# Kernel tuning notes

Measured on AMD Instinct MI355X. Metric: run time of the kernel, lower is better.

Reference implementation:

```python
import jax, jax.numpy as jnp
import numpy as np

BOUND = 25   # max decode steps (module's `bound`)
SOS = 1      # start-of-sequence token index


def setup_inputs() -> dict:
    key = jax.random.key(0)
    ks = jax.random.split(key, 8)
    H, A, D, V, S = 1024, 1024, 512, 50257, 128
    def rn(k, shape, s=0.02):
        return jax.random.normal(k, shape, dtype=jnp.float32) * s
    return {
        "hidden": rn(ks[0], (1, 1, H), 1.0),        # [n_layers, batch=1, H]
        "embeddings": rn(ks[1], (1, S, A), 1.0),    # encoder states [1, S, A]
        "E": rn(ks[2], (V, D)),                      # word embedding table
        "W_ih": rn(ks[3], (3 * H, D)),               # GRU input weights (r,z,n)
        "W_hh": rn(ks[4], (3 * H, H)),               # GRU hidden weights
        "b_ih": jnp.zeros((3 * H,), jnp.float32),
        "b_hh": jnp.zeros((3 * H,), jnp.float32),
        "Wq": rn(ks[5], (A, H)),                     # attention query projection H->A
        "Wout": rn(ks[6], (V, A + H)),               # output projection
        "bout": jnp.zeros((V,), jnp.float32),
    }


def _decode(hidden, embeddings, E, W_ih, W_hh, b_ih, b_hh, Wq, Wout, bout):
    h0 = hidden[-1]  # [1, H] — last-layer hidden (n_layers=1)

    def step(carry, _):
        h, word = carry                      # h: [1,H], word: [1] int32
        x = E[word]                          # [1, D]  (dropout = identity at eval)
        gi = x @ W_ih.T + b_ih               # [1, 3H]
        gh = h @ W_hh.T + b_hh               # [1, 3H]
        ir, iz, inn = jnp.split(gi, 3, axis=-1)
        hr, hz, hn = jnp.split(gh, 3, axis=-1)
        r = jax.nn.sigmoid(ir + hr)
        z = jax.nn.sigmoid(iz + hz)
        n = jnp.tanh(inn + r * hn)
        h_new = (1.0 - z) * n + z * h        # GRU cell (torch gate order r,z,n)
        q = h_new @ Wq.T                     # [1, A] attention query
        scores = jnp.einsum('bsa,ba->bs', embeddings, q)      # [1, S]
        w = jax.nn.softmax(scores, axis=-1)
        attn = jnp.einsum('bs,bsa->ba', w, embeddings)        # [1, A]
        merge = jnp.concatenate([h_new, attn], axis=-1)       # [1, H+A]
        lp = jax.nn.log_softmax(merge @ Wout.T + bout, axis=-1)  # [1, V]
        nw = jnp.argmax(lp, axis=-1).astype(jnp.int32)        # greedy (topk k=1)
        return (h_new, nw), (lp[0], w[0], nw[0])

    word0 = jnp.array([SOS], dtype=jnp.int32)
    _, (log_probs, weights, tokens) = jax.lax.scan(step, (h0, word0), None, length=BOUND)
    # log_probs: [BOUND, V], weights: [BOUND, S], tokens: [BOUND]
    return log_probs, weights, tokens


def reference(hidden, embeddings, E, W_ih, W_hh, b_ih, b_hh, Wq, Wout, bout):
    return _decode(hidden, embeddings, E, W_ih, W_hh, b_ih, b_hh, Wq, Wout, bout)
```

## Files before the change

### kernel.cpp

```cpp
#include <hip/hip_runtime.h>
#include <hip/hip_fp16.h>
#include <math.h>

#define Hh 1024
#define Dd 512
#define Aa 1024
#define Vv 50257
#define Ss 128
#define NSTEP 25

#define OFF_H      0
#define OFF_GI     1024
#define OFF_GH     4096
#define OFF_MERGE  7168
#define OFF_Q      9216
#define OFF_LOGITS 10368
#define OFF_PM     60625
#define OFF_PL     60689
#define OFF_PI     60753
#define OFF_WORD   60818

#define WOUTH_BYTE_OFF (1u << 20)
#define NG_CONV (50257u * 256u)

__global__ void k_conv(const float4* __restrict__ src, uint4* __restrict__ dst, unsigned n8) {
    unsigned stride = gridDim.x * blockDim.x;
    for (unsigned g = blockIdx.x * blockDim.x + threadIdx.x; g < n8; g += stride) {
        float4 a = src[(size_t)g * 2], b = src[(size_t)g * 2 + 1];
        union { __half2 h[4]; uint4 u; } pk;
        pk.h[0] = __float22half2_rn(make_float2(a.x, a.y));
        pk.h[1] = __float22half2_rn(make_float2(a.z, a.w));
        pk.h[2] = __float22half2_rn(make_float2(b.x, b.y));
        pk.h[3] = __float22half2_rn(make_float2(b.z, b.w));
        dst[g] = pk.u;
    }
}

__global__ void k_init(const float* __restrict__ hidden, float* __restrict__ ws) {
    int i = blockIdx.x * blockDim.x + threadIdx.x;
    if (i < Hh) ws[OFF_H + i] = hidden[i];
    if (i == 0) ((int*)ws)[OFF_WORD] = 1;
}

__global__ void k_gates(const float* __restrict__ E, const float* __restrict__ W_ih,
                        const float* __restrict__ W_hh, const float* __restrict__ b_ih,
                        const float* __restrict__ b_hh, float* __restrict__ ws) {
    int gwave = (blockIdx.x * blockDim.x + threadIdx.x) >> 6;
    int lane = threadIdx.x & 63;
    if (gwave >= 3 * Hh) return;
    int word = ((const int*)ws)[OFF_WORD];
    const float4* x  = (const float4*)(E + (size_t)word * Dd);
    const float4* h  = (const float4*)(ws + OFF_H);
    const float4* wi = (const float4*)(W_ih + (size_t)gwave * Dd);
    const float4* wh = (const float4*)(W_hh + (size_t)gwave * Hh);
    float accI = 0.f, accH = 0.f;
    #pragma unroll
    for (int it = 0; it < 2; it++) {
        int k = it * 64 + lane;
        float4 a = wi[k], b = x[k];
        accI += a.x * b.x + a.y * b.y + a.z * b.z + a.w * b.w;
    }
    #pragma unroll
    for (int it = 0; it < 4; it++) {
        int k = it * 64 + lane;
        float4 a = wh[k], b = h[k];
        accH += a.x * b.x + a.y * b.y + a.z * b.z + a.w * b.w;
    }
    for (int off = 32; off; off >>= 1) {
        accI += __shfl_down(accI, off);
        accH += __shfl_down(accH, off);
    }
    if (lane == 0) {
        ws[OFF_GI + gwave] = accI + b_ih[gwave];
        ws[OFF_GH + gwave] = accH + b_hh[gwave];
    }
}

__global__ void k_update(float* __restrict__ ws) {
    int i = blockIdx.x * blockDim.x + threadIdx.x;
    if (i >= Hh) return;
    float ir = ws[OFF_GI + i], iz = ws[OFF_GI + Hh + i], inn = ws[OFF_GI + 2 * Hh + i];
    float hr = ws[OFF_GH + i], hz = ws[OFF_GH + Hh + i], hn  = ws[OFF_GH + 2 * Hh + i];
    float r = 1.f / (1.f + expf(-(ir + hr)));
    float z = 1.f / (1.f + expf(-(iz + hz)));
    float n = tanhf(inn + r * hn);
    float h = ws[OFF_H + i];
    float hnew = (1.f - z) * n + z * h;
    ws[OFF_H + i] = hnew;
    ws[OFF_MERGE + i] = hnew;
}

__global__ void k_query(const float* __restrict__ Wq, float* __restrict__ ws) {
    int gwave = (blockIdx.x * blockDim.x + threadIdx.x) >> 6;
    int lane = threadIdx.x & 63;
    if (gwave >= Aa) return;
    const float4* h = (const float4*)(ws + OFF_H);
    const float4* w = (const float4*)(Wq + (size_t)gwave * Hh);
    float acc = 0.f;
    #pragma unroll
    for (int it = 0; it < 4; it++) {
        int k = it * 64 + lane;
        float4 a = w[k], b = h[k];
        acc += a.x * b.x + a.y * b.y + a.z * b.z + a.w * b.w;
    }
    for (int off = 32; off; off >>= 1) acc += __shfl_down(acc, off);
    if (lane == 0) ws[OFF_Q + gwave] = acc;
}

__global__ void k_scores_attn(const float* __restrict__ emb, float* __restrict__ ws,
                              float* __restrict__ outw) {
    __shared__ float sc[Ss];
    __shared__ float red[4];
    int t = threadIdx.x, wave = t >> 6, lane = t & 63;
    const float4* q = (const float4*)(ws + OFF_Q);
    for (int s = wave; s < Ss; s += 4) {
        const float4* e = (const float4*)(emb + (size_t)s * Aa);
        float acc = 0.f;
        #pragma unroll
        for (int it = 0; it < 4; it++) {
            int k = it * 64 + lane;
            float4 a = e[k], b = q[k];
            acc += a.x * b.x + a.y * b.y + a.z * b.z + a.w * b.w;
        }
        for (int off = 32; off; off >>= 1) acc += __shfl_down(acc, off);
        if (lane == 0) sc[s] = acc;
    }
    __syncthreads();
    float v = (t < Ss) ? sc[t] : -1e30f;
    float m = v;
    for (int off = 32; off; off >>= 1) m = fmaxf(m, __shfl_down(m, off));
    if (lane == 0) red[wave] = m;
    __syncthreads();
    float mm = fmaxf(fmaxf(red[0], red[1]), fmaxf(red[2], red[3]));
    __syncthreads();
    float e = (t < Ss) ? expf(v - mm) : 0.f;
    float sum = e;
    for (int off = 32; off; off >>= 1) sum += __shfl_down(sum, off);
    if (lane == 0) red[wave] = sum;
    __syncthreads();
    float ssum = red[0] + red[1] + red[2] + red[3];
    __syncthreads();
    if (t < Ss) {
        float w = e / ssum;
        sc[t] = w;
        outw[t] = w;
    }
    __syncthreads();
    for (int a = t; a < Aa; a += 256) {
        float acc = 0.f;
        for (int s = 0; s < Ss; s++) acc += sc[s] * emb[(size_t)s * Aa + a];
        ws[OFF_MERGE + Hh + a] = acc;
    }
}

__global__ void k_logits(const uint4* __restrict__ WoutH, const float* __restrict__ bout,
                         float* __restrict__ ws) {
    __shared__ float4 sm[512];
    const float4* mg = (const float4*)(ws + OFF_MERGE);
    for (int i = threadIdx.x; i < 512; i += blockDim.x) sm[i] = mg[i];
    __syncthreads();
    int wave = threadIdx.x >> 6, lane = threadIdx.x & 63;
    int row = blockIdx.x * 4 + wave;
    if (row >= Vv) return;
    const uint4* wr = WoutH + (size_t)row * 256;
    float acc = 0.f;
    #pragma unroll
    for (int it = 0; it < 4; it++) {
        int k = it * 64 + lane;
        union { uint4 u; __half2 h[4]; } pk;
        pk.u = wr[k];
        float4 m0 = sm[k * 2], m1 = sm[k * 2 + 1];
        float2 f0 = __half22float2(pk.h[0]);
        float2 f1 = __half22float2(pk.h[1]);
        float2 f2 = __half22float2(pk.h[2]);
        float2 f3 = __half22float2(pk.h[3]);
        acc += f0.x * m0.x + f0.y * m0.y + f1.x * m0.z + f1.y * m0.w
             + f2.x * m1.x + f2.y * m1.y + f3.x * m1.z + f3.y * m1.w;
    }
    for (int off = 32; off; off >>= 1) acc += __shfl_down(acc, off);
    if (lane == 0) ws[OFF_LOGITS + row] = acc + bout[row];
}

__global__ void k_reduce1(float* __restrict__ ws) {
    const float* logits = ws + OFF_LOGITS;
    __shared__ float smax[256], ssum[256];
    __shared__ int sidx[256];
    int t = threadIdx.x;
    int gid = blockIdx.x * 256 + t;
    float m = -1e30f, l = 0.f;
    int idx = 0;
    for (int i = gid; i < Vv; i += 64 * 256) {
        float v = logits[i];
        if (v > m) { l = l * expf(m - v) + 1.f; m = v; idx = i; }
        else       { l += expf(v - m); }
    }
    smax[t] = m; ssum[t] = l; sidx[t] = idx;
    __syncthreads();
    for (int stride = 128; stride; stride >>= 1) {
        if (t < stride) {
            float m1 = smax[t], l1 = ssum[t]; int i1 = sidx[t];
            float m2 = smax[t + stride], l2 = ssum[t + stride]; int i2 = sidx[t + stride];
            float M = fmaxf(m1, m2);
            float L = l1 * expf(m1 - M) + l2 * expf(m2 - M);
            int I = (m2 > m1) ? i2 : ((m2 < m1) ? i1 : min(i1, i2));
            smax[t] = M; ssum[t] = L; sidx[t] = I;
        }
        __syncthreads();
    }
    if (t == 0) {
        ws[OFF_PM + blockIdx.x] = smax[0];
        ws[OFF_PL + blockIdx.x] = ssum[0];
        ((int*)ws)[OFF_PI + blockIdx.x] = sidx[0];
    }
}

__global__ void k_final(float* __restrict__ ws, float* __restrict__ out_lp,
                        float* __restrict__ out_tok) {
    __shared__ float s_lse;
    int t = threadIdx.x;
    if (t < 64) {
        float m = ws[OFF_PM + t];
        float l = ws[OFF_PL + t];
        int idx = ((const int*)ws)[OFF_PI + t];
        for (int off = 32; off; off >>= 1) {
            float m2 = __shfl_down(m, off);
            float l2 = __shfl_down(l, off);
            int   i2 = __shfl_down(idx, off);
            float M = fmaxf(m, m2);
            float L = l * expf(m - M) + l2 * expf(m2 - M);
            int   I = (m2 > m) ? i2 : ((m2 < m) ? idx : min(idx, i2));
            m = M; l = L; idx = I;
        }
        if (t == 0) {
            s_lse = m + logf(l);
            if (blockIdx.x == 0) {
                ((int*)ws)[OFF_WORD] = idx;
                out_tok[0] = (float)idx;
            }
        }
    }
    __syncthreads();
    int i = blockIdx.x * 256 + t;
    if (i < Vv) out_lp[i] = ws[OFF_LOGITS + i] - s_lse;
}

extern "C" void kernel_launch(void* const* d_in, const int* in_sizes, int n_in,
                              void* d_out, int out_size, void* d_ws, size_t ws_size,
                              hipStream_t stream) {
    const float* hidden = (const float*)d_in[0];
    const float* emb    = (const float*)d_in[1];
    const float* E      = (const float*)d_in[2];
    const float* W_ih   = (const float*)d_in[3];
    const float* W_hh   = (const float*)d_in[4];
    const float* b_ih   = (const float*)d_in[5];
    const float* b_hh   = (const float*)d_in[6];
    const float* Wq     = (const float*)d_in[7];
    const float* Wout   = (const float*)d_in[8];
    const float* bout   = (const float*)d_in[9];

    float* ws = (float*)d_ws;
    uint4* WoutH = (uint4*)((char*)d_ws + WOUTH_BYTE_OFF);
    float* out_lp  = (float*)d_out;
    float* out_w   = out_lp + (size_t)NSTEP * Vv;
    float* out_tok = out_w + (size_t)NSTEP * Ss;

    k_conv<<<8192, 256, 0, stream>>>((const float4*)Wout, WoutH, NG_CONV);
    k_init<<<4, 256, 0, stream>>>(hidden, ws);
    for (int t = 0; t < NSTEP; t++) {
        k_gates      <<<768, 256, 0, stream>>>(E, W_ih, W_hh, b_ih, b_hh, ws);
        k_update     <<<4, 256, 0, stream>>>(ws);
        k_query      <<<256, 256, 0, stream>>>(Wq, ws);
        k_scores_attn<<<1, 256, 0, stream>>>(emb, ws, out_w + (size_t)t * Ss);
        k_logits     <<<(Vv + 3) / 4, 256, 0, stream>>>((const uint4*)WoutH, bout, ws);
        k_reduce1    <<<64, 256, 0, stream>>>(ws);
        k_final      <<<(Vv + 255) / 256, 256, 0, stream>>>(ws, out_lp + (size_t)t * Vv,
                                                            out_tok + t);
    }
}
```

Measured before the change: 2.503 ms.

## Fuse decode step kernels, fold Wq into encoder states, defer log-softmax normalization

Collapses the seven per-step kernels into three. The GRU gates and update are fused into one head kernel that also finishes the previous step's argmax/LSE reduction. The attention query projection is folded into a precomputed emb·Wq matrix, and the attention kernel is spread over eight blocks. Logits are written directly to the output with per-block online max/sum/argmax, and the LSE subtraction runs once for all steps in a final fixup kernel. This cuts launch count, drops one matmul per step and removes the separate logits buffer pass. The trade-offs are the extra one-time fold and fixup kernels, and the head kernel's reduction being redundantly computed by all 256 blocks.

```diff
diff --git a/kernel.cpp b/kernel.cpp
--- a/kernel.cpp
+++ b/kernel.cpp
@@ -9,19 +9,24 @@
 #define Ss 128
 #define NSTEP 25
 
-#define OFF_H      0
-#define OFF_GI     1024
-#define OFF_GH     4096
-#define OFF_MERGE  7168
-#define OFF_Q      9216
-#define OFF_LOGITS 10368
-#define OFF_PM     60625
-#define OFF_PL     60689
-#define OFF_PI     60753
-#define OFF_WORD   60818
+#define ROWS_PER_BLK 16
+#define NBLK_LOG ((Vv + ROWS_PER_BLK - 1) / ROWS_PER_BLK)
+
+#define OFF_H0     0
+#define OFF_H1     1024
+#define OFF_MERGE  2048
+#define OFF_PM     4096
+#define OFF_PL     8192
+#define OFF_PI     12288
+#define OFF_LSE    16384
+#define OFF_M      32768
 
 #define WOUTH_BYTE_OFF (1u << 20)
 #define NG_CONV (50257u * 256u)
+
+__device__ __forceinline__ float dot4(float4 a, float4 b) {
+    return a.x * b.x + a.y * b.y + a.z * b.z + a.w * b.w;
+}
 
 __global__ void k_conv(const float4* __restrict__ src, uint4* __restrict__ dst, unsigned n8) {
     unsigned stride = gridDim.x * blockDim.x;
@@ -36,212 +41,306 @@
     }
 }
 
+__global__ void k_fold(const float* __restrict__ emb, const float* __restrict__ Wq,
+                       float* __restrict__ ws) {
+    __shared__ float se[Aa];
+    int s = blockIdx.x;
+    for (int a = threadIdx.x; a < Aa; a += 256) se[a] = emb[(size_t)s * Aa + a];
+    __syncthreads();
+    int h = threadIdx.x;
+    float a0 = 0.f, a1 = 0.f, a2 = 0.f, a3 = 0.f;
+    for (int a = 0; a < Aa; a++) {
+        float e = se[a];
+        const float* wr = Wq + (size_t)a * Hh;
+        a0 += e * wr[h];
+        a1 += e * wr[h + 256];
+        a2 += e * wr[h + 512];
+        a3 += e * wr[h + 768];
+    }
+    float* Mrow = ws + OFF_M + (size_t)s * Hh;
+    Mrow[h] = a0; Mrow[h + 256] = a1; Mrow[h + 512] = a2; Mrow[h + 768] = a3;
+}
+
 __global__ void k_init(const float* __restrict__ hidden, float* __restrict__ ws) {
     int i = blockIdx.x * blockDim.x + threadIdx.x;
-    if (i < Hh) ws[OFF_H + i] = hidden[i];
-    if (i == 0) ((int*)ws)[OFF_WORD] = 1;
-}
-
-__global__ void k_gates(const float* __restrict__ E, const float* __restrict__ W_ih,
-                        const float* __restrict__ W_hh, const float* __restrict__ b_ih,
-                        const float* __restrict__ b_hh, float* __restrict__ ws) {
-    int gwave = (blockIdx.x * blockDim.x + threadIdx.x) >> 6;
-    int lane = threadIdx.x & 63;
-    if (gwave >= 3 * Hh) return;
-    int word = ((const int*)ws)[OFF_WORD];
-    const float4* x  = (const float4*)(E + (size_t)word * Dd);
-    const float4* h  = (const float4*)(ws + OFF_H);
-    const float4* wi = (const float4*)(W_ih + (size_t)gwave * Dd);
-    const float4* wh = (const float4*)(W_hh + (size_t)gwave * Hh);
-    float accI = 0.f, accH = 0.f;
+    if (i < Hh) ws[OFF_H0 + i] = hidden[i];
+}
+
+__global__ void k_head(int first, int par, int tprev,
+                       const float* __restrict__ E, const float* __restrict__ W_ih,
+                       const float* __restrict__ W_hh, const float* __restrict__ b_ih,
+                       const float* __restrict__ b_hh, float* __restrict__ ws,
+                       float* __restrict__ out_tok) {
+    __shared__ float sm_[256], sl_[256];
+    __shared__ int si_[256];
+    __shared__ int s_word;
+    int t = threadIdx.x;
+    int word;
+    if (first) {
+        word = 1;
+    } else {
+        const float* pm = ws + OFF_PM;
+        const float* pl = ws + OFF_PL;
+        const int* pi = (const int*)ws + OFF_PI;
+        float m = -1e30f, l = 0.f; int idx = 0x7fffffff;
+        for (int i = t; i < NBLK_LOG; i += 256) {
+            float m2 = pm[i], l2 = pl[i]; int i2 = pi[i];
+            float M = fmaxf(m, m2);
+            float L = l * expf(m - M) + l2 * expf(m2 - M);
+            idx = (m2 > m) ? i2 : ((m2 < m) ? idx : min(idx, i2));
+            m = M; l = L;
+        }
+        sm_[t] = m; sl_[t] = l; si_[t] = idx;
+        __syncthreads();
+        for (int s = 128; s; s >>= 1) {
+            if (t < s) {
+                float m1 = sm_[t], l1 = sl_[t]; int i1 = si_[t];
+                float m2 = sm_[t + s], l2 = sl_[t + s]; int i2 = si_[t + s];
+                float M = fmaxf(m1, m2);
+                sl_[t] = l1 * expf(m1 - M) + l2 * expf(m2 - M);
+                si_[t] = (m2 > m1) ? i2 : ((m2 < m1) ? i1 : min(i1, i2));
+                sm_[t] = M;
+            }
+            __syncthreads();
+        }
+        if (t == 0) {
+            s_word = si_[0];
+            if (blockIdx.x == 0) {
+                out_tok[tprev] = (float)si_[0];
+                ws[OFF_LSE + tprev] = sm_[0] + logf(sl_[0]);
+            }
+        }
+        __syncthreads();
+        word = s_word;
+    }
+
+    int lane = t & 63;
+    int row = blockIdx.x * 4 + (t >> 6);
+    const float* hprev = ws + (par ? OFF_H1 : OFF_H0);
+    float* hnext = ws + (par ? OFF_H0 : OFF_H1);
+    const float4* x4 = (const float4*)(E + (size_t)word * Dd);
+    const float4* h4 = (const float4*)hprev;
+    const float4* wir = (const float4*)(W_ih + (size_t)row * Dd);
+    const float4* wiz = (const float4*)(W_ih + (size_t)(Hh + row) * Dd);
+    const float4* win = (const float4*)(W_ih + (size_t)(2 * Hh + row) * Dd);
+    const float4* whr = (const float4*)(W_hh + (size_t)row * Hh);
+    const float4* whz = (const float4*)(W_hh + (size_t)(Hh + row) * Hh);
+    const float4* whn = (const float4*)(W_hh + (size_t)(2 * Hh + row) * Hh);
+    float aIr = 0.f, aIz = 0.f, aIn = 0.f, aHr = 0.f, aHz = 0.f, aHn = 0.f;
     #pragma unroll
     for (int it = 0; it < 2; it++) {
         int k = it * 64 + lane;
-        float4 a = wi[k], b = x[k];
-        accI += a.x * b.x + a.y * b.y + a.z * b.z + a.w * b.w;
+        float4 b = x4[k];
+        aIr += dot4(wir[k], b); aIz += dot4(wiz[k], b); aIn += dot4(win[k], b);
     }
     #pragma unroll
     for (int it = 0; it < 4; it++) {
         int k = it * 64 + lane;
-        float4 a = wh[k], b = h[k];
-        accH += a.x * b.x + a.y * b.y + a.z * b.z + a.w * b.w;
+        float4 b = h4[k];
+        aHr += dot4(whr[k], b); aHz += dot4(whz[k], b); aHn += dot4(whn[k], b);
     }
     for (int off = 32; off; off >>= 1) {
-        accI += __shfl_down(accI, off);
-        accH += __shfl_down(accH, off);
+        aIr += __shfl_down(aIr, off); aIz += __shfl_down(aIz, off); aIn += __shfl_down(aIn, off);
+        aHr += __shfl_down(aHr, off); aHz += __shfl_down(aHz, off); aHn += __shfl_down(aHn, off);
     }
     if (lane == 0) {
-        ws[OFF_GI + gwave] = accI + b_ih[gwave];
-        ws[OFF_GH + gwave] = accH + b_hh[gwave];
-    }
-}
-
-__global__ void k_update(float* __restrict__ ws) {
-    int i = blockIdx.x * blockDim.x + threadIdx.x;
-    if (i >= Hh) return;
-    float ir = ws[OFF_GI + i], iz = ws[OFF_GI + Hh + i], inn = ws[OFF_GI + 2 * Hh + i];
-    float hr = ws[OFF_GH + i], hz = ws[OFF_GH + Hh + i], hn  = ws[OFF_GH + 2 * Hh + i];
-    float r = 1.f / (1.f + expf(-(ir + hr)));
-    float z = 1.f / (1.f + expf(-(iz + hz)));
-    float n = tanhf(inn + r * hn);
-    float h = ws[OFF_H + i];
-    float hnew = (1.f - z) * n + z * h;
-    ws[OFF_H + i] = hnew;
-    ws[OFF_MERGE + i] = hnew;
-}
-
-__global__ void k_query(const float* __restrict__ Wq, float* __restrict__ ws) {
-    int gwave = (blockIdx.x * blockDim.x + threadIdx.x) >> 6;
-    int lane = threadIdx.x & 63;
-    if (gwave >= Aa) return;
-    const float4* h = (const float4*)(ws + OFF_H);
-    const float4* w = (const float4*)(Wq + (size_t)gwave * Hh);
-    float acc = 0.f;
+        float ir = aIr + b_ih[row], iz = aIz + b_ih[Hh + row], inn = aIn + b_ih[2 * Hh + row];
+        float hr = aHr + b_hh[row], hz = aHz + b_hh[Hh + row], hn = aHn + b_hh[2 * Hh + row];
+        float r = 1.f / (1.f + expf(-(ir + hr)));
+        float z = 1.f / (1.f + expf(-(iz + hz)));
+        float n = tanhf(inn + r * hn);
+        float hv = (1.f - z) * n + z * hprev[row];
+        hnext[row] = hv;
+        ws[OFF_MERGE + row] = hv;
+    }
+}
+
+__global__ void k_attn(const float* __restrict__ emb, float* __restrict__ ws,
+                       float* __restrict__ outw) {
+    __shared__ float sh[Hh];
+    __shared__ float sc[Ss];
+    __shared__ float red[256];
+    int t = threadIdx.x;
+    for (int i = t; i < Hh; i += 256) sh[i] = ws[OFF_MERGE + i];
+    __syncthreads();
+    {
+        int s = t & 127, half = t >> 7;
+        const float4* M4 = (const float4*)(ws + OFF_M + (size_t)s * Hh + half * 512);
+        const float4* h44 = (const float4*)(sh + half * 512);
+        float a0 = 0.f, a1 = 0.f, a2 = 0.f, a3 = 0.f;
+        #pragma unroll
+        for (int k = 0; k < 128; k += 4) {
+            a0 += dot4(M4[k], h44[k]);
+            a1 += dot4(M4[k + 1], h44[k + 1]);
+            a2 += dot4(M4[k + 2], h44[k + 2]);
+            a3 += dot4(M4[k + 3], h44[k + 3]);
+        }
+        red[t] = (a0 + a1) + (a2 + a3);
+    }
+    __syncthreads();
+    if (t < 128) sc[t] = red[t] + red[t + 128];
+    __syncthreads();
+    float v = (t < 128) ? sc[t] : -1e30f;
+    float m = v;
+    for (int off = 32; off; off >>= 1) m = fmaxf(m, __shfl_down(m, off));
+    if ((t & 63) == 0) red[t >> 6] = m;
+    __syncthreads();
+    float mm = fmaxf(fmaxf(red[0], red[1]), fmaxf(red[2], red[3]));
+    __syncthreads();
+    float e = (t < 128) ? expf(v - mm) : 0.f;
+    float sum = e;
+    for (int off = 32; off; off >>= 1) sum += __shfl_down(sum, off);
+    if ((t & 63) == 0) red[t >> 6] = sum;
+    __syncthreads();
+    float ssum = red[0] + red[1] + red[2] + red[3];
+    if (t < 128) {
+        float w = e / ssum;
+        sc[t] = w;
+        if (blockIdx.x == 0) outw[t] = w;
+    }
+    __syncthreads();
+    {
+        int a = blockIdx.x * 128 + (t & 127);
+        int half = t >> 7;
+        const float* eb = emb + (size_t)(half * 64) * Aa + a;
+        const float* scp = sc + half * 64;
+        float a0 = 0.f, a1 = 0.f;
+        #pragma unroll
+        for (int s = 0; s < 64; s += 2) {
+            a0 += scp[s] * eb[(size_t)s * Aa];
+            a1 += scp[s + 1] * eb[(size_t)(s + 1) * Aa];
+        }
+        red[t] = a0 + a1;
+    }
+    __syncthreads();
+    if (t < 128) {
+        int a = blockIdx.x * 128 + t;
+        ws[OFF_MERGE + Hh + a] = red[t] + red[t + 128];
+    }
+}
+
+__global__ void k_logits(const uint4* __restrict__ WoutH, const float* __restrict__ bout,
+                         float* __restrict__ ws, float* __restrict__ lp_out) {
+    __shared__ float4 smg[512];
+    __shared__ float wm[4], wl[4];
+    __shared__ int wi_[4];
+    const float4* mg = (const float4*)(ws + OFF_MERGE);
+    for (int i = threadIdx.x; i < 512; i += 256) smg[i] = mg[i];
+    __syncthreads();
+    int wave = threadIdx.x >> 6, lane = threadIdx.x & 63;
+    int row0 = blockIdx.x * ROWS_PER_BLK + wave * 4;
+    const uint4* w0 = WoutH + (size_t)min(row0 + 0, Vv - 1) * 256;
+    const uint4* w1 = WoutH + (size_t)min(row0 + 1, Vv - 1) * 256;
+    const uint4* w2 = WoutH + (size_t)min(row0 + 2, Vv - 1) * 256;
+    const uint4* w3 = WoutH + (size_t)min(row0 + 3, Vv - 1) * 256;
+    float acc0 = 0.f, acc1 = 0.f, acc2 = 0.f, acc3 = 0.f;
     #pragma unroll
     for (int it = 0; it < 4; it++) {
         int k = it * 64 + lane;
-        float4 a = w[k], b = h[k];
-        acc += a.x * b.x + a.y * b.y + a.z * b.z + a.w * b.w;
-    }
-    for (int off = 32; off; off >>= 1) acc += __shfl_down(acc, off);
-    if (lane == 0) ws[OFF_Q + gwave] = acc;
-}
-
-__global__ void k_scores_attn(const float* __restrict__ emb, float* __restrict__ ws,
-                              float* __restrict__ outw) {
-    __shared__ float sc[Ss];
-    __shared__ float red[4];
-    int t = threadIdx.x, wave = t >> 6, lane = t & 63;
-    const float4* q = (const float4*)(ws + OFF_Q);
-    for (int s = wave; s < Ss; s += 4) {
-        const float4* e = (const float4*)(emb + (size_t)s * Aa);
-        float acc = 0.f;
+        float4 m0 = smg[2 * k], m1 = smg[2 * k + 1];
+        {
+            union { uint4 u; __half2 h[4]; } pk; pk.u = w0[k];
+            float2 f0 = __half22float2(pk.h[0]), f1 = __half22float2(pk.h[1]);
+            float2 f2 = __half22float2(pk.h[2]), f3 = __half22float2(pk.h[3]);
+            acc0 += f0.x * m0.x + f0.y * m0.y + f1.x * m0.z + f1.y * m0.w
+                  + f2.x * m1.x + f2.y * m1.y + f3.x * m1.z + f3.y * m1.w;
+        }
+        {
+            union { uint4 u; __half2 h[4]; } pk; pk.u = w1[k];
+            float2 f0 = __half22float2(pk.h[0]), f1 = __half22float2(pk.h[1]);
+            float2 f2 = __half22float2(pk.h[2]), f3 = __half22float2(pk.h[3]);
+            acc1 += f0.x * m0.x + f0.y * m0.y + f1.x * m0.z + f1.y * m0.w
+                  + f2.x * m1.x + f2.y * m1.y + f3.x * m1.z + f3.y * m1.w;
+        }
+        {
+            union { uint4 u; __half2 h[4]; } pk; pk.u = w2[k];
+            float2 f0 = __half22float2(pk.h[0]), f1 = __half22float2(pk.h[1]);
+            float2 f2 = __half22float2(pk.h[2]), f3 = __half22float2(pk.h[3]);
+            acc2 += f0.x * m0.x + f0.y * m0.y + f1.x * m0.z + f1.y * m0.w
+                  + f2.x * m1.x + f2.y * m1.y + f3.x * m1.z + f3.y * m1.w;
+        }
+        {
+            union { uint4 u; __half2 h[4]; } pk; pk.u = w3[k];
+            float2 f0 = __half22float2(pk.h[0]), f1 = __half22float2(pk.h[1]);
+            float2 f2 = __half22float2(pk.h[2]), f3 = __half22float2(pk.h[3]);
+            acc3 += f0.x * m0.x + f0.y * m0.y + f1.x * m0.z + f1.y * m0.w
+                  + f2.x * m1.x + f2.y * m1.y + f3.x * m1.z + f3.y * m1.w;
+        }
+    }
+    for (int off = 32; off; off >>= 1) {
+        acc0 += __shfl_down(acc0, off); acc1 += __shfl_down(acc1, off);
+        acc2 += __shfl_down(acc2, off); acc3 += __shfl_down(acc3, off);
+    }
+    if (lane == 0) {
+        float m = -1e30f, l = 0.f; int idx = 0x7fffffff;
+        float accs[4] = {acc0, acc1, acc2, acc3};
         #pragma unroll
-        for (int it = 0; it < 4; it++) {
-            int k = it * 64 + lane;
-            float4 a = e[k], b = q[k];
-            acc += a.x * b.x + a.y * b.y + a.z * b.z + a.w * b.w;
-        }
-        for (int off = 32; off; off >>= 1) acc += __shfl_down(acc, off);
-        if (lane == 0) sc[s] = acc;
-    }
-    __syncthreads();
-    float v = (t < Ss) ? sc[t] : -1e30f;
-    float m = v;
-    for (int off = 32; off; off >>= 1) m = fmaxf(m, __shfl_down(m, off));
-    if (lane == 0) red[wave] = m;
-    __syncthreads();
-    float mm = fmaxf(fmaxf(red[0], red[1]), fmaxf(red[2], red[3]));
-    __syncthreads();
-    float e = (t < Ss) ? expf(v - mm) : 0.f;
-    float sum = e;
-    for (int off = 32; off; off >>= 1) sum += __shfl_down(sum, off);
-    if (lane == 0) red[wave] = sum;
-    __syncthreads();
-    float ssum = red[0] + red[1] + red[2] + red[3];
-    __syncthreads();
-    if (t < Ss) {
-        float w = e / ssum;
-        sc[t] = w;
-        outw[t] = w;
-    }
-    __syncthreads();
-    for (int a = t; a < Aa; a += 256) {
-        float acc = 0.f;
-        for (int s = 0; s < Ss; s++) acc += sc[s] * emb[(size_t)s * Aa + a];
-        ws[OFF_MERGE + Hh + a] = acc;
-    }
-}
-
-__global__ void k_logits(const uint4* __restrict__ WoutH, const float* __restrict__ bout,
-                         float* __restrict__ ws) {
-    __shared__ float4 sm[512];
-    const float4* mg = (const float4*)(ws + OFF_MERGE);
-    for (int i = threadIdx.x; i < 512; i += blockDim.x) sm[i] = mg[i];
-    __syncthreads();
-    int wave = threadIdx.x >> 6, lane = threadIdx.x & 63;
-    int row = blockIdx.x * 4 + wave;
-    if (row >= Vv) return;
-    const uint4* wr = WoutH + (size_t)row * 256;
-    float acc = 0.f;
-    #pragma unroll
-    for (int it = 0; it < 4; it++) {
-        int k = it * 64 + lane;
-        union { uint4 u; __half2 h[4]; } pk;
-        pk.u = wr[k];
-        float4 m0 = sm[k * 2], m1 = sm[k * 2 + 1];
-        float2 f0 = __half22float2(pk.h[0]);
-        float2 f1 = __half22float2(pk.h[1]);
-        float2 f2 = __half22float2(pk.h[2]);
-        float2 f3 = __half22float2(pk.h[3]);
-        acc += f0.x * m0.x + f0.y * m0.y + f1.x * m0.z + f1.y * m0.w
-             + f2.x * m1.x + f2.y * m1.y + f3.x * m1.z + f3.y * m1.w;
-    }
-    for (int off = 32; off; off >>= 1) acc += __shfl_down(acc, off);
-    if (lane == 0) ws[OFF_LOGITS + row] = acc + bout[row];
-}
-
-__global__ void k_reduce1(float* __restrict__ ws) {
-    const float* logits = ws + OFF_LOGITS;
-    __shared__ float smax[256], ssum[256];
-    __shared__ int sidx[256];
+        for (int r = 0; r < 4; r++) {
+            int row = row0 + r;
+            if (row < Vv) {
+                float v = accs[r] + bout[row];
+                lp_out[row] = v;
+                if (v > m) { l = l * expf(m - v) + 1.f; m = v; idx = row; }
+                else       { l += expf(v - m); }
+            }
+        }
+        wm[wave] = m; wl[wave] = l; wi_[wave] = idx;
+    }
+    __syncthreads();
+    if (threadIdx.x == 0) {
+        float m = wm[0], l = wl[0]; int idx = wi_[0];
+        #pragma unroll
+        for (int wv = 1; wv < 4; wv++) {
+            float m2 = wm[wv], l2 = wl[wv]; int i2 = wi_[wv];
+            float M = fmaxf(m, m2);
+            l = l * expf(m - M) + l2 * expf(m2 - M);
+            idx = (m2 > m) ? i2 : ((m2 < m) ? idx : min(idx, i2));
+            m = M;
+        }
+        ws[OFF_PM + blockIdx.x] = m;
+        ws[OFF_PL + blockIdx.x] = l;
+        ((int*)ws)[OFF_PI + blockIdx.x] = idx;
+    }
+}
+
+__global__ void k_tail(float* __restrict__ ws, float* __restrict__ out_tok) {
+    __shared__ float sm_[256], sl_[256];
+    __shared__ int si_[256];
     int t = threadIdx.x;
-    int gid = blockIdx.x * 256 + t;
-    float m = -1e30f, l = 0.f;
-    int idx = 0;
-    for (int i = gid; i < Vv; i += 64 * 256) {
-        float v = logits[i];
-        if (v > m) { l = l * expf(m - v) + 1.f; m = v; idx = i; }
-        else       { l += expf(v - m); }
-    }
-    smax[t] = m; ssum[t] = l; sidx[t] = idx;
-    __syncthreads();
-    for (int stride = 128; stride; stride >>= 1) {
-        if (t < stride) {
-            float m1 = smax[t], l1 = ssum[t]; int i1 = sidx[t];
-            float m2 = smax[t + stride], l2 = ssum[t + stride]; int i2 = sidx[t + stride];
+    const float* pm = ws + OFF_PM;
+    const float* pl = ws + OFF_PL;
+    const int* pi = (const int*)ws + OFF_PI;
+    float m = -1e30f, l = 0.f; int idx = 0x7fffffff;
+    for (int i = t; i < NBLK_LOG; i += 256) {
+        float m2 = pm[i], l2 = pl[i]; int i2 = pi[i];
+        float M = fmaxf(m, m2);
+        float L = l * expf(m - M) + l2 * expf(m2 - M);
+        idx = (m2 > m) ? i2 : ((m2 < m) ? idx : min(idx, i2));
+        m = M; l = L;
+    }
+    sm_[t] = m; sl_[t] = l; si_[t] = idx;
+    __syncthreads();
+    for (int s = 128; s; s >>= 1) {
+        if (t < s) {
+            float m1 = sm_[t], l1 = sl_[t]; int i1 = si_[t];
+            float m2 = sm_[t + s], l2 = sl_[t + s]; int i2 = si_[t + s];
             float M = fmaxf(m1, m2);
-            float L = l1 * expf(m1 - M) + l2 * expf(m2 - M);
-            int I = (m2 > m1) ? i2 : ((m2 < m1) ? i1 : min(i1, i2));
-            smax[t] = M; ssum[t] = L; sidx[t] = I;
+            sl_[t] = l1 * expf(m1 - M) + l2 * expf(m2 - M);
+            si_[t] = (m2 > m1) ? i2 : ((m2 < m1) ? i1 : min(i1, i2));
+            sm_[t] = M;
         }
         __syncthreads();
     }
     if (t == 0) {
-        ws[OFF_PM + blockIdx.x] = smax[0];
-        ws[OFF_PL + blockIdx.x] = ssum[0];
-        ((int*)ws)[OFF_PI + blockIdx.x] = sidx[0];
-    }
-}
-
-__global__ void k_final(float* __restrict__ ws, float* __restrict__ out_lp,
-                        float* __restrict__ out_tok) {
-    __shared__ float s_lse;
-    int t = threadIdx.x;
-    if (t < 64) {
-        float m = ws[OFF_PM + t];
-        float l = ws[OFF_PL + t];
-        int idx = ((const int*)ws)[OFF_PI + t];
-        for (int off = 32; off; off >>= 1) {
-            float m2 = __shfl_down(m, off);
-            float l2 = __shfl_down(l, off);
-            int   i2 = __shfl_down(idx, off);
-            float M = fmaxf(m, m2);
-            float L = l * expf(m - M) + l2 * expf(m2 - M);
-            int   I = (m2 > m) ? i2 : ((m2 < m) ? idx : min(idx, i2));
-            m = M; l = L; idx = I;
-        }
-        if (t == 0) {
-            s_lse = m + logf(l);
-            if (blockIdx.x == 0) {
-                ((int*)ws)[OFF_WORD] = idx;
-                out_tok[0] = (float)idx;
-            }
-        }
-    }
-    __syncthreads();
-    int i = blockIdx.x * 256 + t;
-    if (i < Vv) out_lp[i] = ws[OFF_LOGITS + i] - s_lse;
+        out_tok[NSTEP - 1] = (float)si_[0];
+        ws[OFF_LSE + NSTEP - 1] = sm_[0] + logf(sl_[0]);
+    }
+}
+
+__global__ void k_fixup(const float* __restrict__ ws, float* __restrict__ out_lp) {
+    int ts = blockIdx.y;
+    int i = blockIdx.x * 256 + threadIdx.x;
+    if (i < Vv) out_lp[(size_t)ts * Vv + i] -= ws[OFF_LSE + ts];
 }
 
 extern "C" void kernel_launch(void* const* d_in, const int* in_sizes, int n_in,
@@ -265,15 +364,15 @@
     float* out_tok = out_w + (size_t)NSTEP * Ss;
 
     k_conv<<<8192, 256, 0, stream>>>((const float4*)Wout, WoutH, NG_CONV);
+    k_fold<<<Ss, 256, 0, stream>>>(emb, Wq, ws);
     k_init<<<4, 256, 0, stream>>>(hidden, ws);
     for (int t = 0; t < NSTEP; t++) {
-        k_gates      <<<768, 256, 0, stream>>>(E, W_ih, W_hh, b_ih, b_hh, ws);
-        k_update     <<<4, 256, 0, stream>>>(ws);
-        k_query      <<<256, 256, 0, stream>>>(Wq, ws);
-        k_scores_attn<<<1, 256, 0, stream>>>(emb, ws, out_w + (size_t)t * Ss);
-        k_logits     <<<(Vv + 3) / 4, 256, 0, stream>>>((const uint4*)WoutH, bout, ws);
-        k_reduce1    <<<64, 256, 0, stream>>>(ws);
-        k_final      <<<(Vv + 255) / 256, 256, 0, stream>>>(ws, out_lp + (size_t)t * Vv,
-                                                            out_tok + t);
-    }
-}
+        k_head  <<<256, 256, 0, stream>>>(t == 0 ? 1 : 0, t & 1, t - 1,
+                                          E, W_ih, W_hh, b_ih, b_hh, ws, out_tok);
+        k_attn  <<<8, 256, 0, stream>>>(emb, ws, out_w + (size_t)t * Ss);
+        k_logits<<<NBLK_LOG, 256, 0, stream>>>((const uint4*)WoutH, bout, ws,
+                                               out_lp + (size_t)t * Vv);
+    }
+    k_tail <<<1, 256, 0, stream>>>(ws, out_tok);
+    k_fixup<<<dim3((Vv + 255) / 256, NSTEP), 256, 0, stream>>>(ws, out_lp);
+}
```

New measurement: 2.608 ms. 1.04x slower.
